# Kernel tuning notes

Measured on AMD Instinct MI355X. Metric: run time of the kernel, lower is better.

The kernel has to match this reference:

```python
import jax, jax.numpy as jnp
import numpy as np

UNITS = 128
D_FEAT = 128
B, N = 4, 4096
EDGE_PROB = 0.01  # avg in-degree ~ N * EDGE_PROB ~ 41


def setup_inputs() -> dict:
    key = jax.random.key(0)
    k1, k2, k3, k4 = jax.random.split(key, 4)
    x = jax.random.normal(k1, (B, N, D_FEAT), dtype=jnp.float32)
    # binary adjacency mask, as consumed by tf.where(adj)
    adj = (jax.random.uniform(k2, (B, N, N)) < EDGE_PROB).astype(jnp.float32)
    # Dense(units, use_bias=False) kernels: msg on concat(x_snd, x_rec) -> [2d, U];
    # node_update on concat(x, messages) -> [d+U, U]
    W_msg = (jax.random.normal(k3, (2 * D_FEAT, UNITS), dtype=jnp.float32)
             / np.sqrt(2 * D_FEAT).astype(np.float32))
    W_upd = (jax.random.normal(k4, (D_FEAT + UNITS, UNITS), dtype=jnp.float32)
             / np.sqrt(D_FEAT + UNITS).astype(np.float32))
    return {"x": x, "adj": adj, "W_msg": W_msg, "W_upd": W_upd}


def reference(x, adj, W_msg, W_upd):
    # Faithful to MPNN2.call: edges are (b, s, r) where adj[b, s, r] != 0.
    # message per edge = concat(x[b,s], x[b,r]) @ W_msg = x[b,s]@Ws + x[b,r]@Wr.
    # messages[b,r] = segment_mean over incoming edges. Since the receiver term
    # x[b,r]@Wr is identical for all edges into r, its mean is itself, and the
    # sender term's mean is (adj^T @ (x@Ws)) / in_degree. Empty segments -> 0
    # (tf.math.unsorted_segment_mean semantics). This avoids data-dependent
    # edge-list shapes and is jit-compatible.
    d = x.shape[-1]
    Ws, Wr = W_msg[:d], W_msg[d:]          # [d, U] each
    xs = x @ Ws                            # sender contribution  [B, N, U]
    xr = x @ Wr                            # receiver contribution [B, N, U]
    deg = jnp.einsum('bsr->br', adj)[..., None]          # in-degree [B, N, 1]
    snd_sum = jnp.einsum('bsr,bsu->bru', adj, xs)        # [B, N, U]
    messages = jnp.where(deg > 0,
                         snd_sum / jnp.maximum(deg, 1.0) + xr,
                         0.0)
    # node_update on concat(x, messages); activation=None, use_bias=False
    return jnp.concatenate([x, messages], axis=-1) @ W_upd
```

## Files before the change

kernel.cpp:

```cpp
#include <hip/hip_runtime.h>

#define BB 4
#define NN 4096
#define ROWS (BB*NN)

typedef __attribute__((ext_vector_type(8))) short short8;
typedef __attribute__((ext_vector_type(4))) float f32x4;

__device__ __forceinline__ unsigned short f2bf(float f) {
    union { float f; unsigned int i; } cv; cv.f = f;
    unsigned int i = cv.i;
    return (unsigned short)((i + 0x7FFFu + ((i >> 16) & 1u)) >> 16);
}

__global__ __launch_bounds__(128) void fold_weights(const float* __restrict__ Wmsg,
                                                    const float* __restrict__ Wupd,
                                                    unsigned short* __restrict__ WcatT) {
    __shared__ float ldsS[128], ldsR[128];
    int k = blockIdx.x, t = threadIdx.x;
    ldsS[t] = Wmsg[k * 128 + t];
    ldsR[t] = Wmsg[(128 + k) * 128 + t];
    __syncthreads();
    float a1 = 0.f, a2 = 0.f;
#pragma unroll 8
    for (int m = 0; m < 128; ++m) {
        float wu = Wupd[(128 + m) * 128 + t];
        a1 += ldsS[m] * wu;
        a2 += ldsR[m] * wu;
    }
    WcatT[(size_t)t * 128 + k]         = f2bf(Wupd[k * 128 + t]);
    WcatT[(size_t)(128 + t) * 128 + k] = f2bf(a2);
    WcatT[(size_t)(256 + t) * 128 + k] = f2bf(a1);
}

__global__ __launch_bounds__(256) void gemm_mfma(const float* __restrict__ X,
                                                 const unsigned short* __restrict__ WcatT,
                                                 float* __restrict__ TD,
                                                 unsigned short* __restrict__ YBT) {
    __shared__ unsigned short Al[64][136];
    __shared__ unsigned short Bl[128][136];
    int t  = threadIdx.x;
    int m0 = blockIdx.x * 64;
    int nb = blockIdx.y;

    {
        int m = t >> 2, seg = t & 3;
        const float* src = X + (size_t)(m0 + m) * 128 + seg * 32;
#pragma unroll
        for (int i = 0; i < 8; ++i) {
            float4 v = *(const float4*)(src + i * 4);
            ushort4 p;
            p.x = f2bf(v.x); p.y = f2bf(v.y); p.z = f2bf(v.z); p.w = f2bf(v.w);
            *(ushort4*)&Al[m][seg * 32 + i * 4] = p;
        }
    }
    {
        int n = t >> 1, half = t & 1;
        const unsigned short* src = WcatT + (size_t)(nb * 128 + n) * 128 + half * 64;
#pragma unroll
        for (int i = 0; i < 8; ++i) {
            uint4 v = *(const uint4*)(src + i * 8);
            *(uint4*)&Bl[n][half * 64 + i * 8] = v;
        }
    }
    __syncthreads();

    int lane = t & 63, wave = t >> 6;
    int quad = lane >> 4, lr = lane & 15;
    int wm = wave * 16;
    f32x4 acc[8];
#pragma unroll
    for (int s = 0; s < 8; ++s) acc[s] = (f32x4)0.f;

#pragma unroll
    for (int kk = 0; kk < 4; ++kk) {
        short8 a = *(short8*)&Al[wm + lr][kk * 32 + quad * 8];
#pragma unroll
        for (int s = 0; s < 8; ++s) {
            short8 bf = *(short8*)&Bl[s * 16 + lr][kk * 32 + quad * 8];
            acc[s] = __builtin_amdgcn_mfma_f32_16x16x32_bf16(a, bf, acc[s], 0, 0, 0);
        }
    }

    if (nb == 2) {
        int b = m0 >> 12;
        int s_base = (m0 & (NN - 1)) + wm + quad * 4;
#pragma unroll
        for (int s = 0; s < 8; ++s) {
            int n = s * 16 + lr;
            ushort4 p;
            p.x = f2bf(acc[s][0]); p.y = f2bf(acc[s][1]);
            p.z = f2bf(acc[s][2]); p.w = f2bf(acc[s][3]);
            *(ushort4*)&YBT[(((size_t)(b << 7) + n) << 12) + s_base] = p;
        }
    } else {
#pragma unroll
        for (int s = 0; s < 8; ++s)
#pragma unroll
            for (int r = 0; r < 4; ++r) {
                int row = m0 + wm + quad * 4 + r;
                TD[(size_t)row * 256 + nb * 128 + s * 16 + lr] = acc[s][r];
            }
    }
}

#define RT 32
#define KT 128
#define NT (NN/KT)
__global__ __launch_bounds__(256) void spmm_out(const float* __restrict__ adj,
                                                const unsigned short* __restrict__ YBT,
                                                const float* __restrict__ TD,
                                                float* __restrict__ out) {
    __shared__ unsigned short At[RT][KT + 8];
    __shared__ float degp[8][RT];
    __shared__ float deg_s[RT];

    int t  = threadIdx.x;
    int r0 = blockIdx.x * RT;
    int b  = blockIdx.y;
    const float* adj_b = adj + (size_t)b * NN * NN;

    int r  = t & 31;
    int kg = t >> 5;
    float va[16];
    float dpart = 0.f;

    int lane = t & 63, wave = t >> 6;
    int wr = wave & 1, wn = wave >> 1;
    int quad = lane >> 4, lr = lane & 15;
    const unsigned short* ybt = YBT + ((size_t)b << 19);

    f32x4 acc0 = (f32x4)0.f, acc1 = (f32x4)0.f, acc2 = (f32x4)0.f, acc3 = (f32x4)0.f;

    {
        const float* p = adj_b + (size_t)(kg * 16) * NN + r0 + r;
#pragma unroll
        for (int j = 0; j < 16; ++j) va[j] = p[(size_t)j * NN];
    }

    for (int tt = 0; tt < NT; ++tt) {
        __syncthreads();
        short8 w0, w1;
#pragma unroll
        for (int j = 0; j < 8; ++j) {
            w0[j] = (short)f2bf(va[j]);
            w1[j] = (short)f2bf(va[j + 8]);
            dpart += va[j] + va[j + 8];
        }
        *(short8*)&At[r][kg * 16]     = w0;
        *(short8*)&At[r][kg * 16 + 8] = w1;
        __syncthreads();
        if (tt + 1 < NT) {
            const float* p = adj_b + (size_t)((tt + 1) * KT + kg * 16) * NN + r0 + r;
#pragma unroll
            for (int j = 0; j < 16; ++j) va[j] = p[(size_t)j * NN];
        }
        int k0 = tt * KT;
#pragma unroll
        for (int kk = 0; kk < 4; ++kk) {
            short8 a = *(short8*)&At[wr * 16 + lr][kk * 32 + quad * 8];
            const unsigned short* bp = ybt + (((size_t)(wn * 64 + lr)) << 12) + k0 + kk * 32 + quad * 8;
            short8 b0 = *(const short8*)(bp);
            short8 b1 = *(const short8*)(bp + (16 << 12));
            short8 b2 = *(const short8*)(bp + (32 << 12));
            short8 b3 = *(const short8*)(bp + (48 << 12));
            acc0 = __builtin_amdgcn_mfma_f32_16x16x32_bf16(a, b0, acc0, 0, 0, 0);
            acc1 = __builtin_amdgcn_mfma_f32_16x16x32_bf16(a, b1, acc1, 0, 0, 0);
            acc2 = __builtin_amdgcn_mfma_f32_16x16x32_bf16(a, b2, acc2, 0, 0, 0);
            acc3 = __builtin_amdgcn_mfma_f32_16x16x32_bf16(a, b3, acc3, 0, 0, 0);
        }
    }

    __syncthreads();
    degp[kg][r] = dpart;
    __syncthreads();
    if (t < RT) {
        float s = 0.f;
#pragma unroll
        for (int g = 0; g < 8; ++g) s += degp[g][t];
        deg_s[t] = s;
    }
    __syncthreads();

    const float* td = TD + ((size_t)(b * NN + r0)) * 256;
    float* ob = out + ((size_t)(b * NN + r0)) * 128;
#pragma unroll
    for (int sf = 0; sf < 4; ++sf) {
        f32x4 a = (sf == 0) ? acc0 : (sf == 1) ? acc1 : (sf == 2) ? acc2 : acc3;
        int n = wn * 64 + sf * 16 + lr;
#pragma unroll
        for (int rr = 0; rr < 4; ++rr) {
            int rl = wr * 16 + quad * 4 + rr;
            float deg = deg_s[rl];
            float v = td[(size_t)rl * 256 + n];
            if (deg > 0.f)
                v += td[(size_t)rl * 256 + 128 + n] + a[rr] / deg;
            ob[(size_t)rl * 128 + n] = v;
        }
    }
}

extern "C" void kernel_launch(void* const* d_in, const int* in_sizes, int n_in,
                              void* d_out, int out_size, void* d_ws, size_t ws_size,
                              hipStream_t stream) {
    const float* x    = (const float*)d_in[0];
    const float* adj  = (const float*)d_in[1];
    const float* Wmsg = (const float*)d_in[2];
    const float* Wupd = (const float*)d_in[3];
    float* out = (float*)d_out;

    char* ws = (char*)d_ws;
    unsigned short* WcatT = (unsigned short*)(ws);
    float*          TD    = (float*)(ws + 131072);
    unsigned short* YBT   = (unsigned short*)(ws + 131072 + 16777216);

    fold_weights<<<128, 128, 0, stream>>>(Wmsg, Wupd, WcatT);
    gemm_mfma<<<dim3(256, 3), 256, 0, stream>>>(x, WcatT, TD, YBT);
    spmm_out<<<dim3(NN / RT, BB), 256, 0, stream>>>(adj, YBT, TD, out);
}
```

Baseline: 462.8 us.

## Bit-pack adjacency and split-K the aggregation with a separate reduction pass

Adds a pass that compresses the float adjacency into per-row bitmasks with wave ballots. The aggregation kernel is restructured into a split-K MFMA over 256-row tiles that expands bits to bf16 in swizzled LDS, writes fp32 partial sums and partial degrees, and a new reduce kernel combines them with the dense terms. The YBT transpose store in the GEMM now goes through LDS so global writes are coalesced. The aim is to replace the strided, repeated fp32 adjacency reads in the old SpMM with a single coalesced sweep and to raise parallelism. In exchange it adds about 64MB of partial-sum traffic and two extra launches.

```diff
diff --git a/kernel.cpp b/kernel.cpp
--- a/kernel.cpp
+++ b/kernel.cpp
@@ -3,6 +3,9 @@
 #define BB 4
 #define NN 4096
 #define ROWS (BB*NN)
+#define KC 8
+#define KCH (NN/KC)
+#define KT 64
 
 typedef __attribute__((ext_vector_type(8))) short short8;
 typedef __attribute__((ext_vector_type(4))) float f32x4;
@@ -11,6 +14,32 @@
     union { float f; unsigned int i; } cv; cv.f = f;
     unsigned int i = cv.i;
     return (unsigned short)((i + 0x7FFFu + ((i >> 16) & 1u)) >> 16);
+}
+
+__global__ __launch_bounds__(256) void pack_bits(const float* __restrict__ adj,
+                                                 unsigned long long* __restrict__ bitT) {
+    int t  = threadIdx.x;
+    int bi = blockIdx.x;
+    int b  = bi >> 7;
+    int s0 = (bi & 127) * 32;
+    int wv = t >> 6, l = t & 63;
+    const float* ab = adj + ((size_t)b * NN + s0) * NN;
+    for (int i = 0; i < 32; ++i) {
+        const float* row = ab + (size_t)i * NN + wv * 1024;
+#pragma unroll
+        for (int it = 0; it < 4; ++it) {
+            float4 v = *(const float4*)(row + it * 256 + l * 4);
+            unsigned long long m0 = __ballot(v.x != 0.0f);
+            unsigned long long m1 = __ballot(v.y != 0.0f);
+            unsigned long long m2 = __ballot(v.z != 0.0f);
+            unsigned long long m3 = __ballot(v.w != 0.0f);
+            if (l < 4) {
+                unsigned long long w = (l == 0) ? m0 : (l == 1) ? m1 : (l == 2) ? m2 : m3;
+                int g = wv * 4 + it;
+                bitT[((size_t)(b * NN + s0 + i) << 6) + g * 4 + l] = w;
+            }
+        }
+    }
 }
 
 __global__ __launch_bounds__(128) void fold_weights(const float* __restrict__ Wmsg,
@@ -37,8 +66,11 @@
                                                  const unsigned short* __restrict__ WcatT,
                                                  float* __restrict__ TD,
                                                  unsigned short* __restrict__ YBT) {
-    __shared__ unsigned short Al[64][136];
-    __shared__ unsigned short Bl[128][136];
+    __shared__ __align__(16) char smem[18432 + 34816];
+    unsigned short (*Al)[136] = (unsigned short (*)[136])smem;
+    unsigned short (*Bl)[136] = (unsigned short (*)[136])(smem + 18432);
+    unsigned short (*Tl)[72]  = (unsigned short (*)[72])smem;
+
     int t  = threadIdx.x;
     int m0 = blockIdx.x * 64;
     int nb = blockIdx.y;
@@ -83,16 +115,24 @@
     }
 
     if (nb == 2) {
-        int b = m0 >> 12;
-        int s_base = (m0 & (NN - 1)) + wm + quad * 4;
+        __syncthreads();
 #pragma unroll
         for (int s = 0; s < 8; ++s) {
             int n = s * 16 + lr;
-            ushort4 p;
-            p.x = f2bf(acc[s][0]); p.y = f2bf(acc[s][1]);
-            p.z = f2bf(acc[s][2]); p.w = f2bf(acc[s][3]);
-            *(ushort4*)&YBT[(((size_t)(b << 7) + n) << 12) + s_base] = p;
-        }
+            unsigned int p0 = (unsigned int)f2bf(acc[s][0]) | ((unsigned int)f2bf(acc[s][1]) << 16);
+            unsigned int p1 = (unsigned int)f2bf(acc[s][2]) | ((unsigned int)f2bf(acc[s][3]) << 16);
+            int m = wm + quad * 4;
+            *(unsigned int*)&Tl[n][m]     = p0;
+            *(unsigned int*)&Tl[n][m + 2] = p1;
+        }
+        __syncthreads();
+        int n = t >> 1, half = t & 1;
+        int b = m0 >> 12;
+        int sbase = (m0 & (NN - 1)) + half * 32;
+        const uint4* srcT = (const uint4*)&Tl[n][half * 32];
+        uint4* dst = (uint4*)&YBT[(((size_t)(b << 7) + n) << 12) + sbase];
+#pragma unroll
+        for (int i = 0; i < 4; ++i) dst[i] = srcT[i];
     } else {
 #pragma unroll
         for (int s = 0; s < 8; ++s)
@@ -104,100 +144,112 @@
     }
 }
 
-#define RT 32
-#define KT 128
-#define NT (NN/KT)
-__global__ __launch_bounds__(256) void spmm_out(const float* __restrict__ adj,
-                                                const unsigned short* __restrict__ YBT,
-                                                const float* __restrict__ TD,
-                                                float* __restrict__ out) {
-    __shared__ unsigned short At[RT][KT + 8];
-    __shared__ float degp[8][RT];
-    __shared__ float deg_s[RT];
+__global__ __launch_bounds__(512, 4) void spmm_part(const unsigned long long* __restrict__ bitT,
+                                                    const unsigned short* __restrict__ YBT,
+                                                    float* __restrict__ Spart,
+                                                    float* __restrict__ degPart) {
+    __shared__ unsigned long long bwl64[KCH][4];
+    __shared__ __align__(16) char Atb[256 * 128];
 
     int t  = threadIdx.x;
-    int r0 = blockIdx.x * RT;
-    int b  = blockIdx.y;
-    const float* adj_b = adj + (size_t)b * NN * NN;
-
-    int r  = t & 31;
-    int kg = t >> 5;
-    float va[16];
-    float dpart = 0.f;
-
-    int lane = t & 63, wave = t >> 6;
-    int wr = wave & 1, wn = wave >> 1;
+    int g  = blockIdx.x;
+    int r0 = g * 256;
+    int kc = blockIdx.y;
+    int b  = blockIdx.z;
+
+    {
+        const unsigned long long* src = bitT + ((size_t)(b * NN + kc * KCH) << 6) + g * 4;
+#pragma unroll
+        for (int j = 0; j < 4; ++j)
+            bwl64[t][j] = src[(size_t)t * 64 + j];
+    }
+
+    int r    = t >> 1;
+    int kh   = t & 1;
+    int jj   = r & 3;
+    int sh   = r >> 2;
+    int wsel = jj * 2 + (sh >> 5);
+    int sh5  = sh & 31;
+    const unsigned int* bw32 = (const unsigned int*)bwl64;
+    unsigned int dsum = 0;
+
+    int lane = t & 63, wv = t >> 6;
     int quad = lane >> 4, lr = lane & 15;
-    const unsigned short* ybt = YBT + ((size_t)b << 19);
-
-    f32x4 acc0 = (f32x4)0.f, acc1 = (f32x4)0.f, acc2 = (f32x4)0.f, acc3 = (f32x4)0.f;
-
-    {
-        const float* p = adj_b + (size_t)(kg * 16) * NN + r0 + r;
-#pragma unroll
-        for (int j = 0; j < 16; ++j) va[j] = p[(size_t)j * NN];
-    }
-
-    for (int tt = 0; tt < NT; ++tt) {
-        __syncthreads();
-        short8 w0, w1;
-#pragma unroll
-        for (int j = 0; j < 8; ++j) {
-            w0[j] = (short)f2bf(va[j]);
-            w1[j] = (short)f2bf(va[j + 8]);
-            dpart += va[j] + va[j + 8];
-        }
-        *(short8*)&At[r][kg * 16]     = w0;
-        *(short8*)&At[r][kg * 16 + 8] = w1;
-        __syncthreads();
-        if (tt + 1 < NT) {
-            const float* p = adj_b + (size_t)((tt + 1) * KT + kg * 16) * NN + r0 + r;
-#pragma unroll
-            for (int j = 0; j < 16; ++j) va[j] = p[(size_t)j * NN];
-        }
-        int k0 = tt * KT;
-#pragma unroll
-        for (int kk = 0; kk < 4; ++kk) {
-            short8 a = *(short8*)&At[wr * 16 + lr][kk * 32 + quad * 8];
-            const unsigned short* bp = ybt + (((size_t)(wn * 64 + lr)) << 12) + k0 + kk * 32 + quad * 8;
-            short8 b0 = *(const short8*)(bp);
-            short8 b1 = *(const short8*)(bp + (16 << 12));
-            short8 b2 = *(const short8*)(bp + (32 << 12));
-            short8 b3 = *(const short8*)(bp + (48 << 12));
-            acc0 = __builtin_amdgcn_mfma_f32_16x16x32_bf16(a, b0, acc0, 0, 0, 0);
-            acc1 = __builtin_amdgcn_mfma_f32_16x16x32_bf16(a, b1, acc1, 0, 0, 0);
-            acc2 = __builtin_amdgcn_mfma_f32_16x16x32_bf16(a, b2, acc2, 0, 0, 0);
-            acc3 = __builtin_amdgcn_mfma_f32_16x16x32_bf16(a, b3, acc3, 0, 0, 0);
-        }
-    }
-
-    __syncthreads();
-    degp[kg][r] = dpart;
-    __syncthreads();
-    if (t < RT) {
-        float s = 0.f;
-#pragma unroll
-        for (int g = 0; g < 8; ++g) s += degp[g][t];
-        deg_s[t] = s;
-    }
-    __syncthreads();
-
-    const float* td = TD + ((size_t)(b * NN + r0)) * 256;
-    float* ob = out + ((size_t)(b * NN + r0)) * 128;
-#pragma unroll
-    for (int sf = 0; sf < 4; ++sf) {
-        f32x4 a = (sf == 0) ? acc0 : (sf == 1) ? acc1 : (sf == 2) ? acc2 : acc3;
-        int n = wn * 64 + sf * 16 + lr;
-#pragma unroll
-        for (int rr = 0; rr < 4; ++rr) {
-            int rl = wr * 16 + quad * 4 + rr;
-            float deg = deg_s[rl];
-            float v = td[(size_t)rl * 256 + n];
-            if (deg > 0.f)
-                v += td[(size_t)rl * 256 + 128 + n] + a[rr] / deg;
-            ob[(size_t)rl * 128 + n] = v;
-        }
-    }
+    const unsigned short* yb = YBT + ((size_t)b << 19) + (size_t)kc * KCH;
+
+    f32x4 acc[16];
+#pragma unroll
+    for (int i = 0; i < 16; ++i) acc[i] = (f32x4)0.f;
+
+    for (int step = 0; step < KCH / KT; ++step) {
+        __syncthreads();
+        int sb = step * KT + kh * 32;
+#pragma unroll
+        for (int o = 0; o < 4; ++o) {
+            short8 w;
+#pragma unroll
+            for (int e = 0; e < 8; ++e) {
+                unsigned int word = bw32[(size_t)(sb + o * 8 + e) * 8 + wsel];
+                unsigned int bit  = (word >> sh5) & 1u;
+                dsum += bit;
+                w[e] = bit ? (short)0x3F80 : (short)0;
+            }
+            int kbyte = (kh * 32 + o * 8) * 2;
+            *(short8*)&Atb[r * 128 + (kbyte ^ ((r & 7) << 4))] = w;
+        }
+        __syncthreads();
+#pragma unroll
+        for (int kk = 0; kk < 2; ++kk) {
+            int kbyte = kk * 64 + quad * 16;
+            int ra0 = wv * 32 + lr, ra1 = wv * 32 + 16 + lr;
+            short8 a0 = *(short8*)&Atb[ra0 * 128 + (kbyte ^ ((ra0 & 7) << 4))];
+            short8 a1 = *(short8*)&Atb[ra1 * 128 + (kbyte ^ ((ra1 & 7) << 4))];
+#pragma unroll
+            for (int nf = 0; nf < 8; ++nf) {
+                short8 bv = *(const short8*)(yb + (((size_t)(nf * 16 + lr)) << 12)
+                                             + step * KT + kk * 32 + quad * 8);
+                acc[nf * 2 + 0] = __builtin_amdgcn_mfma_f32_16x16x32_bf16(a0, bv, acc[nf * 2 + 0], 0, 0, 0);
+                acc[nf * 2 + 1] = __builtin_amdgcn_mfma_f32_16x16x32_bf16(a1, bv, acc[nf * 2 + 1], 0, 0, 0);
+            }
+        }
+    }
+
+    float* sp = Spart + ((size_t)kc << 21) + (((size_t)(b * NN + r0)) << 7);
+#pragma unroll
+    for (int fr = 0; fr < 2; ++fr)
+#pragma unroll
+        for (int nf = 0; nf < 8; ++nf) {
+            f32x4 a = acc[nf * 2 + fr];
+#pragma unroll
+            for (int rr = 0; rr < 4; ++rr) {
+                int rl = wv * 32 + fr * 16 + quad * 4 + rr;
+                sp[(size_t)rl * 128 + nf * 16 + lr] = a[rr];
+            }
+        }
+    unsigned int ds2 = dsum + __shfl_xor((int)dsum, 1, 64);
+    if (kh == 0)
+        degPart[((size_t)(kc * BB + b) << 12) + r0 + r] = (float)ds2;
+}
+
+__global__ __launch_bounds__(256) void reduce_out(const float* __restrict__ Spart,
+                                                  const float* __restrict__ degPart,
+                                                  const float* __restrict__ TD,
+                                                  float* __restrict__ out) {
+    int t   = threadIdx.x;
+    int row = blockIdx.x * 2 + (t >> 7);
+    int n   = t & 127;
+    int b   = row >> 12;
+    int r   = row & (NN - 1);
+    float s = 0.f, deg = 0.f;
+#pragma unroll
+    for (int kc = 0; kc < KC; ++kc) {
+        s   += Spart[((size_t)kc << 21) + ((size_t)row << 7) + n];
+        deg += degPart[((size_t)(kc * BB + b) << 12) + r];
+    }
+    float v = TD[(size_t)row * 256 + n];
+    if (deg > 0.f)
+        v += TD[(size_t)row * 256 + 128 + n] + s / deg;
+    out[(size_t)row * 128 + n] = v;
 }
 
 extern "C" void kernel_launch(void* const* d_in, const int* in_sizes, int n_in,
@@ -210,11 +262,16 @@
     float* out = (float*)d_out;
 
     char* ws = (char*)d_ws;
-    unsigned short* WcatT = (unsigned short*)(ws);
-    float*          TD    = (float*)(ws + 131072);
-    unsigned short* YBT   = (unsigned short*)(ws + 131072 + 16777216);
-
+    unsigned short*     WcatT   = (unsigned short*)(ws);
+    float*              TD      = (float*)(ws + 131072);
+    unsigned short*     YBT     = (unsigned short*)(ws + 16908288);
+    unsigned long long* bitT    = (unsigned long long*)(ws + 21102592);
+    float*              Spart   = (float*)(ws + 29491200);
+    float*              degPart = (float*)(ws + 96600064);
+
+    pack_bits<<<512, 256, 0, stream>>>(adj, bitT);
     fold_weights<<<128, 128, 0, stream>>>(Wmsg, Wupd, WcatT);
     gemm_mfma<<<dim3(256, 3), 256, 0, stream>>>(x, WcatT, TD, YBT);
-    spmm_out<<<dim3(NN / RT, BB), 256, 0, stream>>>(adj, YBT, TD, out);
-}
+    spmm_part<<<dim3(16, KC, BB), 512, 0, stream>>>(bitT, YBT, Spart, degPart);
+    reduce_out<<<ROWS / 2, 256, 0, stream>>>(Spart, degPart, TD, out);
+}
```

After: 498.7 us. 7.8% more time.

## Pack adjacency into bitmasks and run SpMM from compact bits

Applied to the files above, without the earlier changes.

A new pack_bits kernel reads the fp32 adjacency once with coalesced row loads and uses wave ballots to compress it into a transposed bit matrix. The SpMM kernel then rebuilds the 0/1 bf16 operand tiles from those bits in LDS, counts in-degree by popcount of the bits, and splits the output columns across two blocks. The YBT epilogue in the GEMM is also staged through LDS so global stores are coalesced. This removes the strided column-wise fp32 adjacency reads and the per-tile conversion, at the cost of an extra pass over adj, more synchronisation inside the SpMM loop, and a duplicated bit-expansion step for each column half.

```diff
diff --git a/kernel.cpp b/kernel.cpp
--- a/kernel.cpp
+++ b/kernel.cpp
@@ -3,6 +3,7 @@
 #define BB 4
 #define NN 4096
 #define ROWS (BB*NN)
+#define SCH 1024
 
 typedef __attribute__((ext_vector_type(8))) short short8;
 typedef __attribute__((ext_vector_type(4))) float f32x4;
@@ -11,6 +12,43 @@
     union { float f; unsigned int i; } cv; cv.f = f;
     unsigned int i = cv.i;
     return (unsigned short)((i + 0x7FFFu + ((i >> 16) & 1u)) >> 16);
+}
+
+__global__ __launch_bounds__(256) void pack_bits(const float* __restrict__ adj,
+                                                 unsigned long long* __restrict__ bitT) {
+    int t  = threadIdx.x;
+    int bi = blockIdx.x;
+    int b  = bi >> 8;
+    int s0 = (bi & 255) * 16;
+    int wv = t >> 6, l = t & 63;
+    const float* ab = adj + ((size_t)b * NN + s0) * NN + wv * 1024 + l * 4;
+    unsigned long long* bt = bitT + ((size_t)(b * NN + s0) << 6);
+
+    auto PROC = [&](float4* v, int row) {
+#pragma unroll
+        for (int it = 0; it < 4; ++it) {
+            unsigned long long m0 = __ballot(v[it].x != 0.0f);
+            unsigned long long m1 = __ballot(v[it].y != 0.0f);
+            unsigned long long m2 = __ballot(v[it].z != 0.0f);
+            unsigned long long m3 = __ballot(v[it].w != 0.0f);
+            if (l < 4) {
+                unsigned long long wd = (l == 0) ? m0 : (l == 1) ? m1 : (l == 2) ? m2 : m3;
+                bt[((size_t)row << 6) + (wv * 4 + it) * 4 + l] = wd;
+            }
+        }
+    };
+
+    for (int i = 0; i < 16; i += 4) {
+        float4 v0[4], v1[4], v2[4], v3[4];
+#pragma unroll
+        for (int it = 0; it < 4; ++it) {
+            v0[it] = *(const float4*)(ab + (size_t)(i + 0) * NN + it * 256);
+            v1[it] = *(const float4*)(ab + (size_t)(i + 1) * NN + it * 256);
+            v2[it] = *(const float4*)(ab + (size_t)(i + 2) * NN + it * 256);
+            v3[it] = *(const float4*)(ab + (size_t)(i + 3) * NN + it * 256);
+        }
+        PROC(v0, i); PROC(v1, i + 1); PROC(v2, i + 2); PROC(v3, i + 3);
+    }
 }
 
 __global__ __launch_bounds__(128) void fold_weights(const float* __restrict__ Wmsg,
@@ -37,8 +75,11 @@
                                                  const unsigned short* __restrict__ WcatT,
                                                  float* __restrict__ TD,
                                                  unsigned short* __restrict__ YBT) {
-    __shared__ unsigned short Al[64][136];
-    __shared__ unsigned short Bl[128][136];
+    __shared__ __align__(16) char smem[18432 + 34816];
+    unsigned short (*Al)[136] = (unsigned short (*)[136])smem;
+    unsigned short (*Bl)[136] = (unsigned short (*)[136])(smem + 18432);
+    unsigned short (*Tl)[72]  = (unsigned short (*)[72])smem;
+
     int t  = threadIdx.x;
     int m0 = blockIdx.x * 64;
     int nb = blockIdx.y;
@@ -83,16 +124,24 @@
     }
 
     if (nb == 2) {
-        int b = m0 >> 12;
-        int s_base = (m0 & (NN - 1)) + wm + quad * 4;
+        __syncthreads();
 #pragma unroll
         for (int s = 0; s < 8; ++s) {
             int n = s * 16 + lr;
-            ushort4 p;
-            p.x = f2bf(acc[s][0]); p.y = f2bf(acc[s][1]);
-            p.z = f2bf(acc[s][2]); p.w = f2bf(acc[s][3]);
-            *(ushort4*)&YBT[(((size_t)(b << 7) + n) << 12) + s_base] = p;
-        }
+            unsigned int p0 = (unsigned int)f2bf(acc[s][0]) | ((unsigned int)f2bf(acc[s][1]) << 16);
+            unsigned int p1 = (unsigned int)f2bf(acc[s][2]) | ((unsigned int)f2bf(acc[s][3]) << 16);
+            int m = wm + quad * 4;
+            *(unsigned int*)&Tl[n][m]     = p0;
+            *(unsigned int*)&Tl[n][m + 2] = p1;
+        }
+        __syncthreads();
+        int n = t >> 1, half = t & 1;
+        int b = m0 >> 12;
+        int sbase = (m0 & (NN - 1)) + half * 32;
+        const uint4* srcT = (const uint4*)&Tl[n][half * 32];
+        uint4* dst = (uint4*)&YBT[(((size_t)(b << 7) + n) << 12) + sbase];
+#pragma unroll
+        for (int i = 0; i < 4; ++i) dst[i] = srcT[i];
     } else {
 #pragma unroll
         for (int s = 0; s < 8; ++s)
@@ -104,99 +153,117 @@
     }
 }
 
-#define RT 32
-#define KT 128
-#define NT (NN/KT)
-__global__ __launch_bounds__(256) void spmm_out(const float* __restrict__ adj,
-                                                const unsigned short* __restrict__ YBT,
-                                                const float* __restrict__ TD,
-                                                float* __restrict__ out) {
-    __shared__ unsigned short At[RT][KT + 8];
-    __shared__ float degp[8][RT];
-    __shared__ float deg_s[RT];
+__global__ __launch_bounds__(256) void spmm_full(const unsigned long long* __restrict__ bitT,
+                                                 const unsigned short* __restrict__ YBT,
+                                                 const float* __restrict__ TD,
+                                                 float* __restrict__ out) {
+    __shared__ unsigned int bits32[SCH];
+    __shared__ __align__(16) unsigned short At[32 * 64];
+    __shared__ float degp[8][33];
+    __shared__ float deg_s[32];
 
     int t  = threadIdx.x;
-    int r0 = blockIdx.x * RT;
-    int b  = blockIdx.y;
-    const float* adj_b = adj + (size_t)b * NN * NN;
-
-    int r  = t & 31;
-    int kg = t >> 5;
-    float va[16];
-    float dpart = 0.f;
-
-    int lane = t & 63, wave = t >> 6;
-    int wr = wave & 1, wn = wave >> 1;
+    int rt = blockIdx.x;
+    int nh = blockIdx.y;
+    int b  = blockIdx.z;
+    int r0 = rt * 32;
+    int g   = rt >> 3;
+    int bsh = (rt & 7) * 8;
+
+    int er = t & 31, ek = t >> 5;
+    int bpos = ((er & 3) << 3) + (er >> 2);
+
+    int lane = t & 63, w = t >> 6;
     int quad = lane >> 4, lr = lane & 15;
-    const unsigned short* ybt = YBT + ((size_t)b << 19);
-
-    f32x4 acc0 = (f32x4)0.f, acc1 = (f32x4)0.f, acc2 = (f32x4)0.f, acc3 = (f32x4)0.f;
-
-    {
-        const float* p = adj_b + (size_t)(kg * 16) * NN + r0 + r;
-#pragma unroll
-        for (int j = 0; j < 16; ++j) va[j] = p[(size_t)j * NN];
-    }
-
-    for (int tt = 0; tt < NT; ++tt) {
-        __syncthreads();
-        short8 w0, w1;
-#pragma unroll
-        for (int j = 0; j < 8; ++j) {
-            w0[j] = (short)f2bf(va[j]);
-            w1[j] = (short)f2bf(va[j + 8]);
-            dpart += va[j] + va[j + 8];
-        }
-        *(short8*)&At[r][kg * 16]     = w0;
-        *(short8*)&At[r][kg * 16 + 8] = w1;
-        __syncthreads();
-        if (tt + 1 < NT) {
-            const float* p = adj_b + (size_t)((tt + 1) * KT + kg * 16) * NN + r0 + r;
-#pragma unroll
-            for (int j = 0; j < 16; ++j) va[j] = p[(size_t)j * NN];
-        }
-        int k0 = tt * KT;
-#pragma unroll
-        for (int kk = 0; kk < 4; ++kk) {
-            short8 a = *(short8*)&At[wr * 16 + lr][kk * 32 + quad * 8];
-            const unsigned short* bp = ybt + (((size_t)(wn * 64 + lr)) << 12) + k0 + kk * 32 + quad * 8;
-            short8 b0 = *(const short8*)(bp);
-            short8 b1 = *(const short8*)(bp + (16 << 12));
-            short8 b2 = *(const short8*)(bp + (32 << 12));
-            short8 b3 = *(const short8*)(bp + (48 << 12));
-            acc0 = __builtin_amdgcn_mfma_f32_16x16x32_bf16(a, b0, acc0, 0, 0, 0);
-            acc1 = __builtin_amdgcn_mfma_f32_16x16x32_bf16(a, b1, acc1, 0, 0, 0);
-            acc2 = __builtin_amdgcn_mfma_f32_16x16x32_bf16(a, b2, acc2, 0, 0, 0);
-            acc3 = __builtin_amdgcn_mfma_f32_16x16x32_bf16(a, b3, acc3, 0, 0, 0);
-        }
-    }
-
-    __syncthreads();
-    degp[kg][r] = dpart;
-    __syncthreads();
-    if (t < RT) {
+    int wrb = (w & 1) << 4;
+    int wnb = (w >> 1) << 5;
+
+    const unsigned short* yb0 = YBT + ((size_t)b << 19)
+                              + (((size_t)(nh * 64 + wnb + lr)) << 12) + quad * 8;
+    const unsigned short* yb1 = yb0 + ((size_t)16 << 12);
+    const unsigned long long* bt = bitT + ((size_t)(b * NN) << 6) + (g << 2);
+
+    unsigned int dcnt = 0;
+    f32x4 acc0 = (f32x4)0.f, acc1 = (f32x4)0.f;
+
+    for (int cs = 0; cs < NN; cs += SCH) {
+        __syncthreads();
+#pragma unroll
+        for (int i = 0; i < SCH / 256; ++i) {
+            int s = t + 256 * i;
+            const uint4* p = (const uint4*)(bt + ((size_t)(cs + s) << 6));
+            uint4 wa = p[0], wb = p[1];
+            unsigned sl0, sl1, sl2, sl3;
+            if (bsh < 32) {
+                sl0 = (wa.x >> bsh) & 0xFFu;
+                sl1 = (wa.z >> bsh) & 0xFFu;
+                sl2 = (wb.x >> bsh) & 0xFFu;
+                sl3 = (wb.z >> bsh) & 0xFFu;
+            } else {
+                int sh = bsh - 32;
+                sl0 = (wa.y >> sh) & 0xFFu;
+                sl1 = (wa.w >> sh) & 0xFFu;
+                sl2 = (wb.y >> sh) & 0xFFu;
+                sl3 = (wb.w >> sh) & 0xFFu;
+            }
+            bits32[s] = sl0 | (sl1 << 8) | (sl2 << 16) | (sl3 << 24);
+        }
+        __syncthreads();
+
+        for (int st = 0; st < SCH / 64; ++st) {
+            int k0 = cs + st * 64;
+            short8 b00 = *(const short8*)(yb0 + k0);
+            short8 b01 = *(const short8*)(yb0 + k0 + 32);
+            short8 b10 = *(const short8*)(yb1 + k0);
+            short8 b11 = *(const short8*)(yb1 + k0 + 32);
+            int sb = st * 64 + ek * 8;
+            short8 wv8;
+#pragma unroll
+            for (int e = 0; e < 8; ++e) {
+                unsigned bit = (bits32[sb + e] >> bpos) & 1u;
+                dcnt += bit;
+                wv8[e] = bit ? (short)0x3F80 : (short)0;
+            }
+            __syncthreads();
+            *(short8*)((char*)At + er * 128 + ((ek * 16) ^ ((er & 7) << 4))) = wv8;
+            __syncthreads();
+            int ra = wrb + lr;
+            short8 a0 = *(short8*)((char*)At + ra * 128 + ((quad * 16)      ^ ((ra & 7) << 4)));
+            short8 a1 = *(short8*)((char*)At + ra * 128 + ((64 + quad * 16) ^ ((ra & 7) << 4)));
+            acc0 = __builtin_amdgcn_mfma_f32_16x16x32_bf16(a0, b00, acc0, 0, 0, 0);
+            acc1 = __builtin_amdgcn_mfma_f32_16x16x32_bf16(a0, b10, acc1, 0, 0, 0);
+            acc0 = __builtin_amdgcn_mfma_f32_16x16x32_bf16(a1, b01, acc0, 0, 0, 0);
+            acc1 = __builtin_amdgcn_mfma_f32_16x16x32_bf16(a1, b11, acc1, 0, 0, 0);
+        }
+    }
+
+    __syncthreads();
+    degp[ek][er] = (float)dcnt;
+    __syncthreads();
+    if (t < 32) {
         float s = 0.f;
 #pragma unroll
-        for (int g = 0; g < 8; ++g) s += degp[g][t];
+        for (int g8 = 0; g8 < 8; ++g8) s += degp[g8][t];
         deg_s[t] = s;
     }
     __syncthreads();
 
     const float* td = TD + ((size_t)(b * NN + r0)) * 256;
     float* ob = out + ((size_t)(b * NN + r0)) * 128;
-#pragma unroll
-    for (int sf = 0; sf < 4; ++sf) {
-        f32x4 a = (sf == 0) ? acc0 : (sf == 1) ? acc1 : (sf == 2) ? acc2 : acc3;
-        int n = wn * 64 + sf * 16 + lr;
-#pragma unroll
-        for (int rr = 0; rr < 4; ++rr) {
-            int rl = wr * 16 + quad * 4 + rr;
-            float deg = deg_s[rl];
-            float v = td[(size_t)rl * 256 + n];
-            if (deg > 0.f)
-                v += td[(size_t)rl * 256 + 128 + n] + a[rr] / deg;
-            ob[(size_t)rl * 128 + n] = v;
-        }
+    int n0 = nh * 64 + wnb + lr;
+#pragma unroll
+    for (int rr = 0; rr < 4; ++rr) {
+        int rl = wrb + quad * 4 + rr;
+        float deg = deg_s[rl];
+        float v0 = td[(size_t)rl * 256 + n0];
+        float v1 = td[(size_t)rl * 256 + n0 + 16];
+        if (deg > 0.f) {
+            float inv = 1.0f / deg;
+            v0 += td[(size_t)rl * 256 + 128 + n0]      + acc0[rr] * inv;
+            v1 += td[(size_t)rl * 256 + 128 + n0 + 16] + acc1[rr] * inv;
+        }
+        ob[(size_t)rl * 128 + n0]      = v0;
+        ob[(size_t)rl * 128 + n0 + 16] = v1;
     }
 }
 
@@ -210,11 +277,13 @@
     float* out = (float*)d_out;
 
     char* ws = (char*)d_ws;
-    unsigned short* WcatT = (unsigned short*)(ws);
-    float*          TD    = (float*)(ws + 131072);
-    unsigned short* YBT   = (unsigned short*)(ws + 131072 + 16777216);
-
+    unsigned short*     WcatT = (unsigned short*)(ws);
+    float*              TD    = (float*)(ws + 131072);
+    unsigned short*     YBT   = (unsigned short*)(ws + 16908288);
+    unsigned long long* bitT  = (unsigned long long*)(ws + 21102592);
+
+    pack_bits<<<1024, 256, 0, stream>>>(adj, bitT);
     fold_weights<<<128, 128, 0, stream>>>(Wmsg, Wupd, WcatT);
     gemm_mfma<<<dim3(256, 3), 256, 0, stream>>>(x, WcatT, TD, YBT);
-    spmm_out<<<dim3(NN / RT, BB), 256, 0, stream>>>(adj, YBT, TD, out);
-}
+    spmm_full<<<dim3(128, 2, BB), 256, 0, stream>>>(bitT, YBT, TD, out);
+}
```

New measurement: 531.3 us. 1.15x slower.
